# Kernel optimization log

Hardware: AMD Instinct MI355X
Metric: run time of the kernel (lower is better)

Reference implementation:

```python
import jax, jax.numpy as jnp
import numpy as np

DIM = 1024
HEADS = 16
HEAD_DIM = DIM // HEADS
SCALE = HEAD_DIM ** -0.5


def setup_inputs() -> dict:
    key = jax.random.key(0)
    k_x, k_qkv, k_ow, k_ob = jax.random.split(key, 4)
    B, N = 4, 2048
    x = jax.random.normal(k_x, (B, N, DIM), dtype=jnp.float32)
    # nn.Linear(dim, 3*dim, bias=False): weight [3*dim, dim]; we store transposed [dim, 3*dim]
    w_qkv = jax.random.normal(k_qkv, (DIM, 3 * DIM), dtype=jnp.float32) * (DIM ** -0.5)
    w_out = jax.random.normal(k_ow, (DIM, DIM), dtype=jnp.float32) * (DIM ** -0.5)
    b_out = jax.random.normal(k_ob, (DIM,), dtype=jnp.float32) * 0.01
    return {"x": x, "w_qkv": w_qkv, "w_out": w_out, "b_out": b_out}


def reference(x, w_qkv, w_out, b_out):
    B, N, D = x.shape
    H, hd = HEADS, HEAD_DIM
    qkv = x @ w_qkv                                  # [B, N, 3D]
    qkv = qkv.reshape(B, N, 3, H, hd).transpose(2, 0, 3, 1, 4)  # [3, B, H, N, hd]
    q, k, v = qkv[0], qkv[1], qkv[2]
    dots = jnp.einsum('bhnd,bhmd->bhnm', q, k) * SCALE  # [B, H, N, N]
    attn = jax.nn.softmax(dots, axis=-1)
    out = jnp.einsum('bhnm,bhmd->bhnd', attn, v)     # [B, H, N, hd]
    out = out.transpose(0, 2, 1, 3).reshape(B, N, D)
    return out @ w_out + b_out
```

## Files before the change

### kernel.cpp

```cpp
#include <hip/hip_runtime.h>
#include <hip/hip_bf16.h>

#define BSZ   4
#define NSEQ  2048
#define DIMM  1024
#define NHEAD 16
#define HD    64
#define N3    (3*DIMM)
#define MTOK  (BSZ*NSEQ)
#define SCALE 0.125f
#define CQ    0.18033688011112042f

typedef __attribute__((ext_vector_type(8))) short    short8;
typedef __attribute__((ext_vector_type(4))) short    short4v;
typedef __attribute__((ext_vector_type(2))) unsigned uint2v;
typedef __attribute__((ext_vector_type(8))) __bf16   bf16x8;
typedef __attribute__((ext_vector_type(4))) float    f32x4;

__device__ inline short f2bf(float f) {
    unsigned u = __builtin_bit_cast(unsigned, f);
    u += 0x7fffu + ((u >> 16) & 1u);
    return (short)(u >> 16);
}

__device__ inline unsigned pack_bf16(float a, float b) {
    unsigned ua = __builtin_bit_cast(unsigned, a) + 0x8000u;
    unsigned ub = __builtin_bit_cast(unsigned, b) + 0x8000u;
    return __builtin_amdgcn_perm(ub, ua, 0x07060302u);
}

__device__ inline float fast_exp2(float x) {
#if __has_builtin(__builtin_amdgcn_exp2f)
    return __builtin_amdgcn_exp2f(x);
#else
    return exp2f(x);
#endif
}

__device__ inline bf16x8 lds_frag(const short* p) {
    return __builtin_bit_cast(bf16x8, *(const short8*)p);
}

__device__ inline bf16x8 glb_frag(const short* p) {
    return __builtin_bit_cast(bf16x8, *(const short8*)p);
}

__device__ inline void gld_lds16(const short* g, short* l) {
    __builtin_amdgcn_global_load_lds(
        (const __attribute__((address_space(1))) void*)g,
        (__attribute__((address_space(3))) void*)l, 16, 0, 0);
}

__global__ __launch_bounds__(256)
void cvt_bf16(const float* __restrict__ src, short* __restrict__ dst, int n8)
{
    int i = blockIdx.x * 256 + threadIdx.x;
    if (i >= n8) return;
    float4 v0 = ((const float4*)src)[i * 2];
    float4 v1 = ((const float4*)src)[i * 2 + 1];
    short8 s = { f2bf(v0.x), f2bf(v0.y), f2bf(v0.z), f2bf(v0.w),
                 f2bf(v1.x), f2bf(v1.y), f2bf(v1.z), f2bf(v1.w) };
    ((short8*)dst)[i] = s;
}

__global__ __launch_bounds__(256)
void transpose_bf16(const float* __restrict__ src, short* __restrict__ dst,
                    int K, int N)
{
    __shared__ float tile[32][33];
    const int n0 = blockIdx.x * 32, k0 = blockIdx.y * 32;
    const int tx = threadIdx.x, ty = threadIdx.y;
    #pragma unroll
    for (int i = 0; i < 4; ++i)
        tile[ty + i * 8][tx] = src[(size_t)(k0 + ty + i * 8) * N + n0 + tx];
    __syncthreads();
    #pragma unroll
    for (int i = 0; i < 4; ++i)
        dst[(size_t)(n0 + ty + i * 8) * K + k0 + tx] = f2bf(tile[tx][ty + i * 8]);
}

#define GEMM_KLOOP(APTR, BPTR)                                                 \
    for (int k0 = 0; k0 < DIMM; k0 += 32) {                                    \
        _Pragma("unroll")                                                      \
        for (int j = 0; j < 2; ++j) {                                          \
            int c = j * 256 + tid;                                             \
            int r = c >> 2, jj = c & 3;                                        \
            int gc = jj ^ ((r >> 1) & 3);                                      \
            gld_lds16(APTR + (size_t)(row0 + r) * DIMM + k0 + gc * 8,          \
                      As + c * 8);                                             \
            gld_lds16(BPTR + (size_t)(col0 + r) * DIMM + k0 + gc * 8,         \
                      Bs + c * 8);                                             \
        }                                                                      \
        __syncthreads();                                                       \
        bf16x8 af[4], bfr[4];                                                  \
        _Pragma("unroll")                                                      \
        for (int mt = 0; mt < 4; ++mt) {                                       \
            int row = wm + mt * 16 + l16;                                      \
            af[mt] = lds_frag(&As[row * 32 + (quad ^ ((row >> 1) & 3)) * 8]);  \
        }                                                                      \
        _Pragma("unroll")                                                      \
        for (int nt = 0; nt < 4; ++nt) {                                       \
            int row = wn + nt * 16 + l16;                                      \
            bfr[nt] = lds_frag(&Bs[row * 32 + (quad ^ ((row >> 1) & 3)) * 8]); \
        }                                                                      \
        _Pragma("unroll")                                                      \
        for (int mt = 0; mt < 4; ++mt)                                         \
            _Pragma("unroll")                                                  \
            for (int nt = 0; nt < 4; ++nt)                                     \
                acc[mt][nt] = __builtin_amdgcn_mfma_f32_16x16x32_bf16(         \
                    af[mt], bfr[nt], acc[mt][nt], 0, 0, 0);                    \
        __syncthreads();                                                       \
    }

__global__ __launch_bounds__(256, 2)
void gemm_qkv(const short* __restrict__ a, const short* __restrict__ bt,
              short* __restrict__ qo, short* __restrict__ ko,
              short* __restrict__ vo)
{
    __shared__ short As[128 * 32];
    __shared__ short Bs[128 * 32];
    const int tid  = threadIdx.x;
    const int wave = tid >> 6, lane = tid & 63;
    const int quad = lane >> 4, l16 = lane & 15;
    const int row0 = blockIdx.x * 128, col0 = blockIdx.y * 128;
    const int wm = (wave >> 1) * 64, wn = (wave & 1) * 64;

    f32x4 acc[4][4] = {};
    GEMM_KLOOP(a, bt)

    #pragma unroll
    for (int mt = 0; mt < 4; ++mt) {
        #pragma unroll
        for (int nt = 0; nt < 4; ++nt) {
            int gcol  = col0 + wn + nt * 16 + l16;
            int which = gcol >> 10;
            int cc    = gcol & 1023;
            int h     = cc >> 6, d = cc & 63;
            int growb = row0 + wm + mt * 16 + quad * 4;
            int b_    = growb >> 11;
            int n_    = growb & 2047;
            int bh    = b_ * NHEAD + h;
            if (which == 2) {
                short4v s = { f2bf(acc[mt][nt][0]), f2bf(acc[mt][nt][1]),
                              f2bf(acc[mt][nt][2]), f2bf(acc[mt][nt][3]) };
                *(short4v*)(vo + ((size_t)bh * HD + d) * NSEQ + n_) = s;
            } else if (which == 0) {
                #pragma unroll
                for (int r = 0; r < 4; ++r)
                    qo[((size_t)bh * NSEQ + n_ + r) * HD + d] =
                        f2bf(acc[mt][nt][r] * CQ);
            } else {
                #pragma unroll
                for (int r = 0; r < 4; ++r)
                    ko[((size_t)bh * NSEQ + n_ + r) * HD + d] = f2bf(acc[mt][nt][r]);
            }
        }
    }
}

__global__ __launch_bounds__(256, 3)
void attn(const short* __restrict__ q, const short* __restrict__ k,
          const short* __restrict__ vt, short* __restrict__ o)
{
    __shared__ short Ks[2][64 * 64];
    __shared__ short Ps[4][32 * 72];

    const int tid  = threadIdx.x;
    const int wave = tid >> 6, lane = tid & 63;
    const int quad = lane >> 4, l16 = lane & 15;
    const int bh   = blockIdx.y;
    const int q0   = blockIdx.x * 128;
    const size_t qkbase = (size_t)bh * NSEQ * HD;
    const size_t vbase  = (size_t)bh * HD * NSEQ;

    bf16x8 qf[2][2];
    #pragma unroll
    for (int g = 0; g < 2; ++g)
        #pragma unroll
        for (int ks = 0; ks < 2; ++ks)
            qf[g][ks] = glb_frag(q + qkbase +
                (size_t)(q0 + wave * 32 + g * 16 + l16) * HD + ks * 32 + quad * 8);

    f32x4 oacc[4][2] = {};
    float lsum[2] = {0.f, 0.f};
    short* Pw = &Ps[wave][0];

    const int  sr   = tid >> 3, sj = tid & 7;
    const int  soff = sr * HD + ((sj ^ (sr & 7)) * 8);
    const short* kbh = k + qkbase;

    gld_lds16(kbh + soff,            &Ks[0][tid * 8]);
    gld_lds16(kbh + soff + 32 * HD,  &Ks[0][2048 + tid * 8]);

    for (int t = 0; t < NSEQ / 64; ++t) {
        const int kv0 = t * 64;
        __syncthreads();
        if (t + 1 < NSEQ / 64) {
            const short* src = kbh + (size_t)(kv0 + 64) * HD;
            short* dst = &Ks[(t + 1) & 1][0];
            gld_lds16(src + soff,           dst + tid * 8);
            gld_lds16(src + soff + 32 * HD, dst + 2048 + tid * 8);
        }
        const short* Kb = &Ks[t & 1][0];

        bf16x8 vf[2][4];
        #pragma unroll
        for (int ks2 = 0; ks2 < 2; ++ks2)
            #pragma unroll
            for (int ot = 0; ot < 4; ++ot)
                vf[ks2][ot] = glb_frag(vt + vbase +
                    (size_t)(ot * 16 + l16) * NSEQ + kv0 + ks2 * 32 + quad * 8);

        f32x4 sacc[4][2] = {};
        #pragma unroll
        for (int nt = 0; nt < 4; ++nt) {
            int row = nt * 16 + l16;
            #pragma unroll
            for (int ks = 0; ks < 2; ++ks) {
                bf16x8 kf = lds_frag(&Kb[row * 64 + (((ks * 4 + quad) ^ (row & 7)) * 8)]);
                #pragma unroll
                for (int g = 0; g < 2; ++g)
                    sacc[nt][g] = __builtin_amdgcn_mfma_f32_16x16x32_bf16(
                        kf, qf[g][ks], sacc[nt][g], 0, 0, 0);
            }
        }

        #pragma unroll
        for (int g = 0; g < 2; ++g) {
            #pragma unroll
            for (int nt = 0; nt < 4; ++nt) {
                float p0 = fast_exp2(sacc[nt][g][0]);
                float p1 = fast_exp2(sacc[nt][g][1]);
                float p2 = fast_exp2(sacc[nt][g][2]);
                float p3 = fast_exp2(sacc[nt][g][3]);
                lsum[g] += (p0 + p1) + (p2 + p3);
                uint2v u = { pack_bf16(p0, p1), pack_bf16(p2, p3) };
                *(uint2v*)&Pw[(g * 16 + l16) * 72 + nt * 16 + quad * 4] = u;
            }
        }

        #pragma unroll
        for (int ks2 = 0; ks2 < 2; ++ks2) {
            bf16x8 pf[2];
            #pragma unroll
            for (int g = 0; g < 2; ++g)
                pf[g] = lds_frag(&Pw[(g * 16 + l16) * 72 + ks2 * 32 + quad * 8]);
            #pragma unroll
            for (int ot = 0; ot < 4; ++ot)
                #pragma unroll
                for (int g = 0; g < 2; ++g)
                    oacc[ot][g] = __builtin_amdgcn_mfma_f32_16x16x32_bf16(
                        vf[ks2][ot], pf[g], oacc[ot][g], 0, 0, 0);
        }
    }

    const int b_ = bh >> 4, h = bh & 15;
    float inv[2];
    #pragma unroll
    for (int g = 0; g < 2; ++g) {
        float l = lsum[g];
        l += __shfl_xor(l, 16);
        l += __shfl_xor(l, 32);
        inv[g] = 1.f / l;
    }
    #pragma unroll
    for (int ot = 0; ot < 4; ++ot) {
        #pragma unroll
        for (int g = 0; g < 2; ++g) {
            short4v s4 = { f2bf(oacc[ot][g][0] * inv[g]),
                           f2bf(oacc[ot][g][1] * inv[g]),
                           f2bf(oacc[ot][g][2] * inv[g]),
                           f2bf(oacc[ot][g][3] * inv[g]) };
            *(short4v*)(o + ((size_t)b_ * NSEQ + q0 + wave * 32 + g * 16 + l16) * DIMM +
                        h * HD + ot * 16 + quad * 4) = s4;
        }
    }
}

__global__ __launch_bounds__(256, 2)
void gemm_out(const short* __restrict__ a, const short* __restrict__ bt,
              const float* __restrict__ bias, float* __restrict__ out)
{
    __shared__ short As[128 * 32];
    __shared__ short Bs[128 * 32];
    const int tid  = threadIdx.x;
    const int wave = tid >> 6, lane = tid & 63;
    const int quad = lane >> 4, l16 = lane & 15;
    const int row0 = blockIdx.x * 128, col0 = blockIdx.y * 128;
    const int wm = (wave >> 1) * 64, wn = (wave & 1) * 64;

    f32x4 acc[4][4] = {};
    GEMM_KLOOP(a, bt)

    #pragma unroll
    for (int mt = 0; mt < 4; ++mt) {
        #pragma unroll
        for (int nt = 0; nt < 4; ++nt) {
            int gcol = col0 + wn + nt * 16 + l16;
            float bb = bias[gcol];
            #pragma unroll
            for (int r = 0; r < 4; ++r) {
                int grow = row0 + wm + mt * 16 + quad * 4 + r;
                out[(size_t)grow * DIMM + gcol] = acc[mt][nt][r] + bb;
            }
        }
    }
}

extern "C" void kernel_launch(void* const* d_in, const int* in_sizes, int n_in,
                              void* d_out, int out_size, void* d_ws, size_t ws_size,
                              hipStream_t stream)
{
    const float* x     = (const float*)d_in[0];
    const float* w_qkv = (const float*)d_in[1];
    const float* w_out = (const float*)d_in[2];
    const float* b_out = (const float*)d_in[3];
    float* out = (float*)d_out;

    const size_t per = (size_t)BSZ * NHEAD * NSEQ * HD;
    short* q     = (short*)d_ws;
    short* kk    = q  + per;
    short* v     = kk + per;
    short* xb_ob = v  + per;
    short* wqkvT = xb_ob + per;
    short* woutT = wqkvT + (size_t)N3 * DIMM;

    cvt_bf16<<<(int)(per / 8 / 256), 256, 0, stream>>>(x, xb_ob, (int)(per / 8));
    transpose_bf16<<<dim3(N3 / 32, DIMM / 32), dim3(32, 8), 0, stream>>>(w_qkv, wqkvT, DIMM, N3);
    transpose_bf16<<<dim3(DIMM / 32, DIMM / 32), dim3(32, 8), 0, stream>>>(w_out, woutT, DIMM, DIMM);

    gemm_qkv<<<dim3(MTOK / 128, N3 / 128), 256, 0, stream>>>(xb_ob, wqkvT, q, kk, v);
    attn<<<dim3(NSEQ / 128, BSZ * NHEAD), 256, 0, stream>>>(q, kk, v, xb_ob);
    gemm_out<<<dim3(MTOK / 128, DIMM / 128), 256, 0, stream>>>(xb_ob, woutT, b_out, out);
}
```

Baseline: 315.0 us.

## Software-pipeline attention loop so PV of previous tile overlaps next QK

Restructures the attention main loop into a prologue, steady state and epilogue. Each iteration now computes QK scores for tile t, then does the PV MMA for tile t-1 using the P values written in the previous iteration, then does the exponentials for tile t. The aim is to let the MFMA work overlap with the exp/pack and LDS traffic, and to hide V global-load latency. It costs extra live registers for a second score accumulator, which could lower occupancy at launch bounds of 3.

Result: slower. 363.3 us (+15.3%).

```diff
diff --git a/kernel.cpp b/kernel.cpp
--- a/kernel.cpp
+++ b/kernel.cpp
@@ -172,6 +172,7 @@
     const int q0   = blockIdx.x * 128;
     const size_t qkbase = (size_t)bh * NSEQ * HD;
     const size_t vbase  = (size_t)bh * HD * NSEQ;
+    const int T = NSEQ / 64;
 
     bf16x8 qf[2][2];
     #pragma unroll
@@ -188,30 +189,75 @@
     const int  sr   = tid >> 3, sj = tid & 7;
     const int  soff = sr * HD + ((sj ^ (sr & 7)) * 8);
     const short* kbh = k + qkbase;
+    const short* vtb = vt + vbase + (size_t)l16 * NSEQ + quad * 8;
 
     gld_lds16(kbh + soff,            &Ks[0][tid * 8]);
     gld_lds16(kbh + soff + 32 * HD,  &Ks[0][2048 + tid * 8]);
 
-    for (int t = 0; t < NSEQ / 64; ++t) {
-        const int kv0 = t * 64;
+    f32x4 sacc[4][2];
+
+    __syncthreads();
+    {
+        const short* src = kbh + (size_t)64 * HD;
+        gld_lds16(src + soff,           &Ks[1][tid * 8]);
+        gld_lds16(src + soff + 32 * HD, &Ks[1][2048 + tid * 8]);
+    }
+    #pragma unroll
+    for (int nt = 0; nt < 4; ++nt)
+        #pragma unroll
+        for (int g = 0; g < 2; ++g)
+            sacc[nt][g] = f32x4{0.f, 0.f, 0.f, 0.f};
+    #pragma unroll
+    for (int nt = 0; nt < 4; ++nt) {
+        int row = nt * 16 + l16;
+        #pragma unroll
+        for (int ks = 0; ks < 2; ++ks) {
+            bf16x8 kf = lds_frag(&Ks[0][row * 64 + (((ks * 4 + quad) ^ (row & 7)) * 8)]);
+            #pragma unroll
+            for (int g = 0; g < 2; ++g)
+                sacc[nt][g] = __builtin_amdgcn_mfma_f32_16x16x32_bf16(
+                    kf, qf[g][ks], sacc[nt][g], 0, 0, 0);
+        }
+    }
+    #pragma unroll
+    for (int g = 0; g < 2; ++g) {
+        #pragma unroll
+        for (int nt = 0; nt < 4; ++nt) {
+            float p0 = fast_exp2(sacc[nt][g][0]);
+            float p1 = fast_exp2(sacc[nt][g][1]);
+            float p2 = fast_exp2(sacc[nt][g][2]);
+            float p3 = fast_exp2(sacc[nt][g][3]);
+            lsum[g] += (p0 + p1) + (p2 + p3);
+            uint2v u = { pack_bf16(p0, p1), pack_bf16(p2, p3) };
+            *(uint2v*)&Pw[(g * 16 + l16) * 72 + nt * 16 + quad * 4] = u;
+        }
+    }
+
+    for (int t = 1; t < T; ++t) {
+        const int kv0  = t * 64;
         __syncthreads();
-        if (t + 1 < NSEQ / 64) {
+        if (t + 1 < T) {
             const short* src = kbh + (size_t)(kv0 + 64) * HD;
             short* dst = &Ks[(t + 1) & 1][0];
             gld_lds16(src + soff,           dst + tid * 8);
             gld_lds16(src + soff + 32 * HD, dst + 2048 + tid * 8);
         }
+
+        bf16x8 vf[2][4];
+        #pragma unroll
+        for (int ks2 = 0; ks2 < 2; ++ks2)
+            #pragma unroll
+            for (int ot = 0; ot < 4; ++ot)
+                vf[ks2][ot] = glb_frag(vtb + (size_t)(ot * 16) * NSEQ +
+                                       (kv0 - 64) + ks2 * 32);
+
         const short* Kb = &Ks[t & 1][0];
-
-        bf16x8 vf[2][4];
-        #pragma unroll
-        for (int ks2 = 0; ks2 < 2; ++ks2)
-            #pragma unroll
-            for (int ot = 0; ot < 4; ++ot)
-                vf[ks2][ot] = glb_frag(vt + vbase +
-                    (size_t)(ot * 16 + l16) * NSEQ + kv0 + ks2 * 32 + quad * 8);
-
-        f32x4 sacc[4][2] = {};
+        f32x4 s2[4][2];
+        #pragma unroll
+        for (int nt = 0; nt < 4; ++nt)
+            #pragma unroll
+            for (int g = 0; g < 2; ++g)
+                s2[nt][g] = f32x4{0.f, 0.f, 0.f, 0.f};
         #pragma unroll
         for (int nt = 0; nt < 4; ++nt) {
             int row = nt * 16 + l16;
@@ -220,38 +266,65 @@
                 bf16x8 kf = lds_frag(&Kb[row * 64 + (((ks * 4 + quad) ^ (row & 7)) * 8)]);
                 #pragma unroll
                 for (int g = 0; g < 2; ++g)
-                    sacc[nt][g] = __builtin_amdgcn_mfma_f32_16x16x32_bf16(
-                        kf, qf[g][ks], sacc[nt][g], 0, 0, 0);
+                    s2[nt][g] = __builtin_amdgcn_mfma_f32_16x16x32_bf16(
+                        kf, qf[g][ks], s2[nt][g], 0, 0, 0);
             }
         }
 
+        bf16x8 pf[2][2];
+        #pragma unroll
+        for (int g = 0; g < 2; ++g)
+            #pragma unroll
+            for (int ks2 = 0; ks2 < 2; ++ks2)
+                pf[g][ks2] = lds_frag(&Pw[(g * 16 + l16) * 72 + ks2 * 32 + quad * 8]);
+
+        #pragma unroll
+        for (int ks2 = 0; ks2 < 2; ++ks2)
+            #pragma unroll
+            for (int ot = 0; ot < 4; ++ot)
+                #pragma unroll
+                for (int g = 0; g < 2; ++g)
+                    oacc[ot][g] = __builtin_amdgcn_mfma_f32_16x16x32_bf16(
+                        vf[ks2][ot], pf[g][ks2], oacc[ot][g], 0, 0, 0);
+
         #pragma unroll
         for (int g = 0; g < 2; ++g) {
             #pragma unroll
             for (int nt = 0; nt < 4; ++nt) {
-                float p0 = fast_exp2(sacc[nt][g][0]);
-                float p1 = fast_exp2(sacc[nt][g][1]);
-                float p2 = fast_exp2(sacc[nt][g][2]);
-                float p3 = fast_exp2(sacc[nt][g][3]);
+                float p0 = fast_exp2(s2[nt][g][0]);
+                float p1 = fast_exp2(s2[nt][g][1]);
+                float p2 = fast_exp2(s2[nt][g][2]);
+                float p3 = fast_exp2(s2[nt][g][3]);
                 lsum[g] += (p0 + p1) + (p2 + p3);
                 uint2v u = { pack_bf16(p0, p1), pack_bf16(p2, p3) };
                 *(uint2v*)&Pw[(g * 16 + l16) * 72 + nt * 16 + quad * 4] = u;
             }
         }
-
-        #pragma unroll
-        for (int ks2 = 0; ks2 < 2; ++ks2) {
-            bf16x8 pf[2];
-            #pragma unroll
-            for (int g = 0; g < 2; ++g)
-                pf[g] = lds_frag(&Pw[(g * 16 + l16) * 72 + ks2 * 32 + quad * 8]);
+    }
+
+    {
+        const int kv0 = (T - 1) * 64;
+        bf16x8 vf[2][4];
+        #pragma unroll
+        for (int ks2 = 0; ks2 < 2; ++ks2)
+            #pragma unroll
+            for (int ot = 0; ot < 4; ++ot)
+                vf[ks2][ot] = glb_frag(vtb + (size_t)(ot * 16) * NSEQ +
+                                       kv0 + ks2 * 32);
+        bf16x8 pf[2][2];
+        #pragma unroll
+        for (int g = 0; g < 2; ++g)
+            #pragma unroll
+            for (int ks2 = 0; ks2 < 2; ++ks2)
+                pf[g][ks2] = lds_frag(&Pw[(g * 16 + l16) * 72 + ks2 * 32 + quad * 8]);
+        #pragma unroll
+        for (int ks2 = 0; ks2 < 2; ++ks2)
             #pragma unroll
             for (int ot = 0; ot < 4; ++ot)
                 #pragma unroll
                 for (int g = 0; g < 2; ++g)
                     oacc[ot][g] = __builtin_amdgcn_mfma_f32_16x16x32_bf16(
-                        vf[ks2][ot], pf[g], oacc[ot][g], 0, 0, 0);
-        }
+                        vf[ks2][ot], pf[g][ks2], oacc[ot][g], 0, 0, 0);
     }
 
     const int b_ = bh >> 4, h = bh & 15;
```

## Swizzle attention P buffer in LDS and retile output GEMM to 64x128

Applied to the files above, without the earlier changes.

The per-wave P staging buffer in the attention kernel changes from a padded 72-short stride to an unpadded 64-short stride with an XOR swizzle on the 8-element column chunk, which reduces LDS use and is meant to avoid bank conflicts. The output projection GEMM drops from 128x128 to 64x128 tiles with its own single-buffered k-loop, doubles its block count, and raises launch bounds to 3 blocks per SM. This gives better occupancy and wave count for the small 8192x1024 GEMM. The cost is less reuse per tile and two barriers per k step with no prefetch.

Measured after the change: 362.2 us. 15.0% more time.

```diff
diff --git a/kernel.cpp b/kernel.cpp
--- a/kernel.cpp
+++ b/kernel.cpp
@@ -163,7 +163,7 @@
           const short* __restrict__ vt, short* __restrict__ o)
 {
     __shared__ short Ks[2][64 * 64];
-    __shared__ short Ps[4][32 * 72];
+    __shared__ short Ps[4][32 * 64];
 
     const int tid  = threadIdx.x;
     const int wave = tid >> 6, lane = tid & 63;
@@ -184,6 +184,7 @@
     f32x4 oacc[4][2] = {};
     float lsum[2] = {0.f, 0.f};
     short* Pw = &Ps[wave][0];
+    const int psw = l16 & 7;
 
     const int  sr   = tid >> 3, sj = tid & 7;
     const int  soff = sr * HD + ((sj ^ (sr & 7)) * 8);
@@ -235,7 +236,8 @@
                 float p3 = fast_exp2(sacc[nt][g][3]);
                 lsum[g] += (p0 + p1) + (p2 + p3);
                 uint2v u = { pack_bf16(p0, p1), pack_bf16(p2, p3) };
-                *(uint2v*)&Pw[(g * 16 + l16) * 72 + nt * 16 + quad * 4] = u;
+                int pc = (nt * 2 + (quad >> 1)) ^ psw;
+                *(uint2v*)&Pw[(g * 16 + l16) * 64 + pc * 8 + (quad & 1) * 4] = u;
             }
         }
 
@@ -244,7 +246,8 @@
             bf16x8 pf[2];
             #pragma unroll
             for (int g = 0; g < 2; ++g)
-                pf[g] = lds_frag(&Pw[(g * 16 + l16) * 72 + ks2 * 32 + quad * 8]);
+                pf[g] = lds_frag(&Pw[(g * 16 + l16) * 64 +
+                                     (((ks2 * 4 + quad) ^ psw) * 8)]);
             #pragma unroll
             for (int ot = 0; ot < 4; ++ot)
                 #pragma unroll
@@ -277,23 +280,56 @@
     }
 }
 
-__global__ __launch_bounds__(256, 2)
+__global__ __launch_bounds__(256, 3)
 void gemm_out(const short* __restrict__ a, const short* __restrict__ bt,
               const float* __restrict__ bias, float* __restrict__ out)
 {
-    __shared__ short As[128 * 32];
+    __shared__ short As[64 * 32];
     __shared__ short Bs[128 * 32];
     const int tid  = threadIdx.x;
     const int wave = tid >> 6, lane = tid & 63;
     const int quad = lane >> 4, l16 = lane & 15;
-    const int row0 = blockIdx.x * 128, col0 = blockIdx.y * 128;
-    const int wm = (wave >> 1) * 64, wn = (wave & 1) * 64;
-
-    f32x4 acc[4][4] = {};
-    GEMM_KLOOP(a, bt)
-
-    #pragma unroll
-    for (int mt = 0; mt < 4; ++mt) {
+    const int row0 = blockIdx.x * 64, col0 = blockIdx.y * 128;
+    const int wm = (wave & 1) * 32, wn = (wave >> 1) * 64;
+
+    f32x4 acc[2][4] = {};
+
+    for (int k0 = 0; k0 < DIMM; k0 += 32) {
+        {
+            int r = tid >> 2, jj = tid & 3;
+            int gc = jj ^ ((r >> 1) & 3);
+            gld_lds16(a + (size_t)(row0 + r) * DIMM + k0 + gc * 8, As + tid * 8);
+        }
+        #pragma unroll
+        for (int j = 0; j < 2; ++j) {
+            int c = j * 256 + tid;
+            int r = c >> 2, jj = c & 3;
+            int gc = jj ^ ((r >> 1) & 3);
+            gld_lds16(bt + (size_t)(col0 + r) * DIMM + k0 + gc * 8, Bs + c * 8);
+        }
+        __syncthreads();
+        bf16x8 af[2], bfr[4];
+        #pragma unroll
+        for (int mt = 0; mt < 2; ++mt) {
+            int row = wm + mt * 16 + l16;
+            af[mt] = lds_frag(&As[row * 32 + (quad ^ ((row >> 1) & 3)) * 8]);
+        }
+        #pragma unroll
+        for (int nt = 0; nt < 4; ++nt) {
+            int row = wn + nt * 16 + l16;
+            bfr[nt] = lds_frag(&Bs[row * 32 + (quad ^ ((row >> 1) & 3)) * 8]);
+        }
+        #pragma unroll
+        for (int mt = 0; mt < 2; ++mt)
+            #pragma unroll
+            for (int nt = 0; nt < 4; ++nt)
+                acc[mt][nt] = __builtin_amdgcn_mfma_f32_16x16x32_bf16(
+                    af[mt], bfr[nt], acc[mt][nt], 0, 0, 0);
+        __syncthreads();
+    }
+
+    #pragma unroll
+    for (int mt = 0; mt < 2; ++mt) {
         #pragma unroll
         for (int nt = 0; nt < 4; ++nt) {
             int gcol = col0 + wn + nt * 16 + l16;
@@ -331,5 +367,5 @@
 
     gemm_qkv<<<dim3(MTOK / 128, N3 / 128), 256, 0, stream>>>(xb_ob, wqkvT, q, kk, v);
     attn<<<dim3(NSEQ / 128, BSZ * NHEAD), 256, 0, stream>>>(q, kk, v, xb_ob);
-    gemm_out<<<dim3(MTOK / 128, DIMM / 128), 256, 0, stream>>>(xb_ob, woutT, b_out, out);
-}
+    gemm_out<<<dim3(MTOK / 64, DIMM / 128), 256, 0, stream>>>(xb_ob, woutT, b_out, out);
+}
```
